# Kernel optimization log

Hardware: AMD Instinct MI355X
Metric: run time of the kernel (lower is better)

Reference implementation:

```python
import jax, jax.numpy as jnp
import numpy as np

B, N, D, H = 8, 1024, 512, 8
DH = D // H  # 64
ALPHA = 0.2  # LeakyReLU slope (args.alpha)
EPS = 1e-6
NEG = -1e9


def layer_norm(x, g, b):
    mean = jnp.mean(x, axis=-1, keepdims=True)
    std = jnp.std(x, axis=-1, keepdims=True)
    return g * (x - mean) / (std + EPS) + b


def setup_inputs() -> dict:
    key = jax.random.key(0)
    ks = jax.random.split(key, 6)
    x = jax.random.normal(ks[0], (B, N, D), dtype=jnp.float32)
    mask = jnp.zeros((B, N), dtype=jnp.int32)  # unused by the block body
    adj = jax.random.randint(ks[1], (B, N, N), 0, 2).astype(jnp.int32)
    W = jax.random.normal(ks[2], (H, D, DH), dtype=jnp.float32) * 0.05
    a_src = jax.random.normal(ks[3], (H, DH), dtype=jnp.float32) * 0.05
    a_dst = jax.random.normal(ks[4], (H, DH), dtype=jnp.float32) * 0.05
    ln1_g = jnp.ones((D,), jnp.float32)
    ln1_b = jnp.zeros((D,), jnp.float32)
    ln2_g = jnp.ones((D,), jnp.float32)
    ln2_b = jnp.zeros((D,), jnp.float32)
    return {"x": x, "mask": mask, "adj": adj, "W": W, "a_src": a_src,
            "a_dst": a_dst, "ln1_g": ln1_g, "ln1_b": ln1_b,
            "ln2_g": ln2_g, "ln2_b": ln2_b}


def ggat(xn, adj, W, a_src, a_dst):
    # multi-head GAT-style attention over dense adjacency (inputP)
    h = jnp.einsum('bnd,hdk->bhnk', xn, W)                 # [B,H,N,DH]
    f_src = jnp.einsum('bhnk,hk->bhn', h, a_src)           # [B,H,N]
    f_dst = jnp.einsum('bhnk,hk->bhn', h, a_dst)
    e = jax.nn.leaky_relu(f_src[..., :, None] + f_dst[..., None, :], ALPHA)
    e = jnp.where(adj[:, None, :, :] > 0, e, NEG)          # mask non-edges
    attn = jax.nn.softmax(e, axis=-1)                      # [B,H,N,N]
    out = jnp.einsum('bhnm,bhmk->bhnk', attn, h)           # aggregate
    out = out.transpose(0, 2, 1, 3).reshape(out.shape[0], out.shape[2], -1)
    return jax.nn.elu(out)                                 # [B,N,D]


def reference(x, mask, adj, W, a_src, a_dst, ln1_g, ln1_b, ln2_g, ln2_b):
    # SublayerConnection: x + dropout(sublayer(norm(x))); dropout = identity (eval)
    xn = layer_norm(x, ln1_g, ln1_b)
    y = x + ggat(xn, adj, W, a_src, a_dst)
    # extra LayerNorm + dropout(identity); module returns (dropout(x), 0)
    y = layer_norm(y, ln2_g, ln2_b)
    return y
```

## Files before the change

kernel.cpp:

```cpp
#include <hip/hip_runtime.h>
#include <stdint.h>

#define B_ 8
#define N_ 1024
#define D_ 512
#define H_ 8
#define DH_ 64


using f16x8 = __attribute__((ext_vector_type(8))) _Float16;
using h2    = __attribute__((ext_vector_type(2))) _Float16;
using f32x4 = __attribute__((ext_vector_type(4))) float;

__device__ __forceinline__ float bf2f(uint32_t u) {
  union { uint32_t u; float f; } c; c.u = u << 16; return c.f;
}
__device__ __forceinline__ uint16_t f2bf(float f) {
  union { float f; uint32_t u; } c; c.f = f;
  return (uint16_t)((c.u + 0x7FFFu + ((c.u >> 16) & 1u)) >> 16);
}
__device__ __forceinline__ uint16_t f2h(float f) {
  union { _Float16 h; uint16_t u; } c; c.h = (_Float16)f; return c.u;
}
__device__ __forceinline__ float h2f(uint16_t u) {
  union { uint16_t u; _Float16 h; } c; c.u = u; return (float)c.h;
}
__device__ __forceinline__ uint32_t pk2h(float a, float b) {
  union { h2 h; uint32_t u; } c; c.h = (h2){(_Float16)a, (_Float16)b}; return c.u;
}
__device__ __forceinline__ h2 u2h2(uint32_t u) {
  union { uint32_t u; h2 h; } c; c.u = u; return c.h;
}
__device__ __forceinline__ uint32_t h22u(h2 h) {
  union { h2 h; uint32_t u; } c; c.h = h; return c.u;
}
__device__ __forceinline__ h2 h2splat(float v) {
  return (h2){(_Float16)v, (_Float16)v};
}
__device__ __forceinline__ h2 hmax2(h2 a, h2 b) {
#if defined(__has_builtin)
#if __has_builtin(__builtin_elementwise_max)
  return __builtin_elementwise_max(a, b);
#else
  h2 r; r.x = a.x > b.x ? a.x : b.x; r.y = a.y > b.y ? a.y : b.y; return r;
#endif
#else
  h2 r; r.x = a.x > b.x ? a.x : b.x; r.y = a.y > b.y ? a.y : b.y; return r;
#endif
}
__device__ __forceinline__ void gload16(const void* g, void* l) {
  __builtin_amdgcn_global_load_lds(
      (const __attribute__((address_space(1))) uint32_t*)g,
      (__attribute__((address_space(3))) uint32_t*)l, 16, 0, 0);
}
__device__ __forceinline__ void load8f(const void* p, size_t idx, int f32, float v[8]) {
  if (f32) {
    const float4* q = (const float4*)((const float*)p + idx);
    float4 a = q[0], b = q[1];
    v[0]=a.x; v[1]=a.y; v[2]=a.z; v[3]=a.w; v[4]=b.x; v[5]=b.y; v[6]=b.z; v[7]=b.w;
  } else {
    uint4 u = *(const uint4*)((const uint16_t*)p + idx);
    const uint32_t* w = (const uint32_t*)&u;
#pragma unroll
    for (int e = 0; e < 4; e++) { v[2*e] = bf2f(w[e] & 0xffffu); v[2*e+1] = bf2f(w[e] >> 16); }
  }
}
__device__ __forceinline__ float load1f(const void* p, size_t idx, int f32) {
  return f32 ? ((const float*)p)[idx] : bf2f(((const uint16_t*)p)[idx]);
}

__device__ __forceinline__ int detect_f32_block(const uint16_t* x, int t, int* sflag) {
  if (t == 0) *sflag = 0;
  __syncthreads();
  uint2 u = ((const uint2*)x)[t];
  uint32_t bad = 0;
  bad |= (((u.x >> 7)  & 0xffu) >= 0x90u);
  bad |= (((u.x >> 23) & 0xffu) >= 0x90u);
  bad |= (((u.y >> 7)  & 0xffu) >= 0x90u);
  bad |= (((u.y >> 23) & 0xffu) >= 0x90u);
  if (__any(bad)) { if ((t & 63) == 0) atomicOr(sflag, 1); }
  __syncthreads();
  return *sflag;
}

__global__ __launch_bounds__(256) void k_pp(const int* __restrict__ adj,
                                            unsigned long long* __restrict__ adjp,
                                            const uint16_t* __restrict__ xr,
                                            int* __restrict__ flag,
                                            const void* __restrict__ x,
                                            const void* __restrict__ g,
                                            const void* __restrict__ bb,
                                            uint16_t* __restrict__ xn,
                                            const void* __restrict__ W,
                                            uint16_t* __restrict__ Wt) {
  const int bx = blockIdx.x, t = threadIdx.x;
  if (bx < 2048) {
    const int row  = bx * 4 + (t >> 6);
    const int lane = t & 63;
    const int* ar = adj + (size_t)row * N_;
#pragma unroll
    for (int c = 0; c < 16; c++) {
      unsigned long long m = __ballot(ar[c * 64 + lane] > 0);
      if (lane == 0) adjp[(size_t)row * 16 + c] = m;
    }
    return;
  }
  __shared__ int sflag;
  if (bx == 2048) {
    int f32 = detect_f32_block(xr, t, &sflag);
    if (t == 0) *flag = f32;
    return;
  }
  if (bx >= 4097) {
    const int f32 = detect_f32_block(xr, t, &sflag);
    const int bw = bx - 4097;
    const int h = bw >> 3, dt = bw & 7;
    __shared__ uint16_t tile[64][65];
    const size_t sbase = ((size_t)h * D_ + dt * 64) * DH_;
    for (int e = t; e < 4096; e += 256) tile[e >> 6][e & 63] = f2h(load1f(W, sbase + e, f32));
    __syncthreads();
    uint16_t* dst = Wt + (size_t)h * DH_ * D_ + dt * 64;
    for (int e = t; e < 4096; e += 256) {
      const int k = e >> 6, dd = e & 63;
      dst[(size_t)k * D_ + dd] = tile[dd][k];
    }
    return;
  }
  const int f32 = detect_f32_block(xr, t, &sflag);
  const int row  = (bx - 2049) * 4 + (t >> 6);
  const int lane = t & 63;
  const size_t base = (size_t)row * D_ + lane * 8;
  float v[8]; load8f(x, base, f32, v);
  float s = 0.f, sq = 0.f;
#pragma unroll
  for (int e = 0; e < 8; e++) { s += v[e]; sq += v[e] * v[e]; }
#pragma unroll
  for (int d = 32; d; d >>= 1) { s += __shfl_xor(s, d); sq += __shfl_xor(sq, d); }
  const float mean = s * (1.0f / D_);
  float var = fmaxf(sq * (1.0f / D_) - mean * mean, 0.0f);
  const float inv = 1.0f / (sqrtf(var) + 1e-6f);
  float gv[8], bv[8];
  load8f(g, lane * 8, f32, gv); load8f(bb, lane * 8, f32, bv);
  uint4 ov; uint32_t* ow = (uint32_t*)&ov;
#pragma unroll
  for (int e = 0; e < 4; e++) {
    float o0 = gv[2*e]   * ((v[2*e]   - mean) * inv) + bv[2*e];
    float o1 = gv[2*e+1] * ((v[2*e+1] - mean) * inv) + bv[2*e+1];
    ow[e] = (uint32_t)f2h(o0) | ((uint32_t)f2h(o1) << 16);
  }
  *(uint4*)(xn + base) = ov;
}

__global__ __launch_bounds__(256, 2) void k_gemm(const uint16_t* __restrict__ xn,
                                              const uint16_t* __restrict__ Wt,
                                              uint16_t* __restrict__ ht,
                                              const void* __restrict__ asr,
                                              const void* __restrict__ adst,
                                              float* __restrict__ fs,
                                              float* __restrict__ fd,
                                              const int* __restrict__ flag) {
  const int h = blockIdx.x;
  const int r0 = blockIdx.y * 64;
  const int t = threadIdx.x;
  const int wv = t >> 6, lane = t & 63, q = lane >> 4, m16 = lane & 15;
  const int wr = wv >> 1, wc = wv & 1;

  __shared__ union {
    struct { __align__(16) uint16_t A[2][64 * 72]; __align__(16) uint16_t Bt[2][64 * 72]; } st;
    __align__(16) uint16_t tr[64 * 72];
  } L;

  f32x4 acc[2][2] = {};
  const int srow = t >> 2, soff = (t & 3) * 16;
  const int o = srow * 72 + soff;
  const uint16_t* gA = xn + (size_t)(r0 + srow) * D_ + soff;
  const uint16_t* gB = Wt + ((size_t)h * DH_ + srow) * D_ + soff;

  uint4 va0 = *(const uint4*)(gA);
  uint4 va1 = *(const uint4*)(gA + 8);
  uint4 vb0 = *(const uint4*)(gB);
  uint4 vb1 = *(const uint4*)(gB + 8);
  *(uint4*)&L.st.A[0][o]      = va0;  *(uint4*)&L.st.A[0][o + 8]  = va1;
  *(uint4*)&L.st.Bt[0][o]     = vb0;  *(uint4*)&L.st.Bt[0][o + 8] = vb1;
  va0 = *(const uint4*)(gA + 64);  va1 = *(const uint4*)(gA + 72);
  vb0 = *(const uint4*)(gB + 64);  vb1 = *(const uint4*)(gB + 72);
  int cur = 0;
  for (int k0 = 0; k0 < D_; k0 += 64) {
    __syncthreads();
    if (k0 + 64 < D_) {
      *(uint4*)&L.st.A[cur ^ 1][o]      = va0;  *(uint4*)&L.st.A[cur ^ 1][o + 8]  = va1;
      *(uint4*)&L.st.Bt[cur ^ 1][o]     = vb0;  *(uint4*)&L.st.Bt[cur ^ 1][o + 8] = vb1;
      if (k0 + 128 < D_) {
        va0 = *(const uint4*)(gA + k0 + 128);  va1 = *(const uint4*)(gA + k0 + 136);
        vb0 = *(const uint4*)(gB + k0 + 128);  vb1 = *(const uint4*)(gB + k0 + 136);
      }
    }
#pragma unroll
    for (int ks = 0; ks < 2; ks++) {
      f16x8 a0 = *(const f16x8*)&L.st.A[cur][(wr * 32 + m16) * 72 + ks * 32 + q * 8];
      f16x8 a1 = *(const f16x8*)&L.st.A[cur][(wr * 32 + 16 + m16) * 72 + ks * 32 + q * 8];
      f16x8 b0 = *(const f16x8*)&L.st.Bt[cur][(wc * 32 + m16) * 72 + ks * 32 + q * 8];
      f16x8 b1 = *(const f16x8*)&L.st.Bt[cur][(wc * 32 + 16 + m16) * 72 + ks * 32 + q * 8];
      acc[0][0] = __builtin_amdgcn_mfma_f32_16x16x32_f16(a0, b0, acc[0][0], 0, 0, 0);
      acc[0][1] = __builtin_amdgcn_mfma_f32_16x16x32_f16(a0, b1, acc[0][1], 0, 0, 0);
      acc[1][0] = __builtin_amdgcn_mfma_f32_16x16x32_f16(a1, b0, acc[1][0], 0, 0, 0);
      acc[1][1] = __builtin_amdgcn_mfma_f32_16x16x32_f16(a1, b1, acc[1][1], 0, 0, 0);
    }
    cur ^= 1;
  }
  __syncthreads();
#pragma unroll
  for (int i2 = 0; i2 < 2; i2++)
#pragma unroll
    for (int j2 = 0; j2 < 2; j2++) {
      f32x4 vv = acc[i2][j2];
      const int sl = wr * 32 + i2 * 16 + q * 4;
      const int kl = wc * 32 + j2 * 16 + m16;
#pragma unroll
      for (int r = 0; r < 4; r++) L.tr[kl * 72 + sl + r] = f2h(vv[r]);
    }
  __syncthreads();
  const int b = r0 >> 10, n0 = r0 & 1023;
  {
    const int k = t >> 2, ns = (t & 3) * 16;
    const size_t base = (((size_t)b * H_ + h) * DH_ + k) * (size_t)N_ + n0 + ns;
    *(uint4*)(ht + base) = *(const uint4*)&L.tr[k * 72 + ns];
    *(uint4*)(ht + base + 8) = *(const uint4*)&L.tr[k * 72 + ns + 8];
  }
  {
    const int f32 = *flag;
    const int nl = t >> 2, qd = (t & 3) * 16;
    float ss = 0.f, sd = 0.f;
#pragma unroll
    for (int dd = 0; dd < 16; dd++) {
      float hv = h2f(L.tr[(qd + dd) * 72 + nl]);
      ss = fmaf(hv, load1f(asr,  h * DH_ + qd + dd, f32), ss);
      sd = fmaf(hv, load1f(adst, h * DH_ + qd + dd, f32), sd);
    }
    ss += __shfl_xor(ss, 1); ss += __shfl_xor(ss, 2);
    sd += __shfl_xor(sd, 1); sd += __shfl_xor(sd, 2);
    if ((t & 3) == 0) {
      fs[((size_t)b * H_ + h) * N_ + n0 + nl] = ss;
      fd[((size_t)b * H_ + h) * N_ + n0 + nl] = sd;
    }
  }
}

__global__ __launch_bounds__(256, 2) void k_attn(const uint16_t* __restrict__ ht,
                                                 const float* __restrict__ fs,
                                                 const float* __restrict__ fd,
                                                 const uint32_t* __restrict__ adjp,
                                                 uint16_t* __restrict__ oat) {
  const int bid = blockIdx.x;
  const int bh = bid & 63, itile = bid >> 6;
  const int b = bh >> 3, h = bh & 7;
  const int i0 = itile * 128;
  const int t = threadIdx.x, wv = t >> 6, lane = t & 63, q = lane >> 4, m16 = lane & 15;
  __shared__ __align__(16) uint16_t Hs[2][64 * 128];
  __shared__ __align__(16) uint32_t E1p[N_ / 2];
  __shared__ __align__(16) uint32_t E2p[N_ / 2];

  const uint16_t* hbase = ht + (size_t)bh * (DH_ * N_);
  int srow[4], soff[4];
#pragma unroll
  for (int i = 0; i < 4; i++) {
    const int r = wv * 16 + i * 4 + (lane >> 4);
    srow[i] = r;
    soff[i] = ((lane & 15) * 8) ^ ((r & 7) << 3);
  }
#define STAGE(jc, buf)                                                         \
  {                                                                            \
    _Pragma("unroll")                                                          \
    for (int ii = 0; ii < 4; ii++) {                                           \
      gload16(hbase + (size_t)srow[ii] * N_ + (jc) + soff[ii],                 \
              &(buf)[(wv * 16 + ii * 4) * 128]);                               \
    }                                                                          \
  }
  STAGE(0, Hs[0]);

  for (int jp = t; jp < N_ / 2; jp += 256) {
    float2 fv = ((const float2*)(fd + (size_t)bh * N_))[jp];
    E1p[jp] = pk2h(exp2f(fv.x * 1.44269504f), exp2f(fv.y * 1.44269504f));
    E2p[jp] = pk2h(exp2f(fv.x * 0.28853901f), exp2f(fv.y * 0.28853901f));
  }
  const int iA0 = i0 + wv * 32 + m16;
  const int iA1 = iA0 + 16;
  const h2 R0 = h2splat(fminf(exp2f(fs[(size_t)bh * N_ + iA0] * -1.15415603f), 60000.f));
  const h2 R1 = h2splat(fminf(exp2f(fs[(size_t)bh * N_ + iA1] * -1.15415603f), 60000.f));
  const uint32_t* arow0 = adjp + ((size_t)b * N_ + iA0) * 32;
  const uint32_t* arow1 = adjp + ((size_t)b * N_ + iA1) * 32;
  union { uint16_t u[8]; f16x8 v; } ones;
#pragma unroll
  for (int e = 0; e < 8; e++) ones.u[e] = 0x3C00u;
  f32x4 acc[2][5] = {};
  const int csw = (m16 & 7) << 3;
  uint4 aw0 = *(const uint4*)(arow0);
  uint4 aw1 = *(const uint4*)(arow1);
  for (int c = 0; c < 8; c++) {
    __syncthreads();
    if (c < 7) STAGE((c + 1) * 128, Hs[(c + 1) & 1]);
    const uint32_t cw0[4] = {aw0.x, aw0.y, aw0.z, aw0.w};
    const uint32_t cw1[4] = {aw1.x, aw1.y, aw1.z, aw1.w};
    if (c < 7) {
      aw0 = *(const uint4*)(arow0 + (c + 1) * 4);
      aw1 = *(const uint4*)(arow1 + (c + 1) * 4);
    }
    const uint16_t* Hc = Hs[c & 1];
    const int eb = c * 64;
#pragma unroll
    for (int s = 0; s < 4; s++) {
      const int js = s * 32;
      const int jb = (js + q * 8) ^ csw;
      f16x8 hf0 = *(const f16x8*)&Hc[(m16)*128      + jb];
      f16x8 hf1 = *(const f16x8*)&Hc[(16 + m16)*128 + jb];
      f16x8 hf2 = *(const f16x8*)&Hc[(32 + m16)*128 + jb];
      f16x8 hf3 = *(const f16x8*)&Hc[(48 + m16)*128 + jb];
      const int ei = eb + s * 16 + q * 4;
      const uint4 e1u = *(const uint4*)&E1p[ei];
      const uint4 e2u = *(const uint4*)&E2p[ei];
      const h2 e1[4] = {u2h2(e1u.x), u2h2(e1u.y), u2h2(e1u.z), u2h2(e1u.w)};
      const h2 e2[4] = {u2h2(e2u.x), u2h2(e2u.y), u2h2(e2u.z), u2h2(e2u.w)};
      const uint32_t ab0 = (cw0[s] >> (q * 8)) & 0xffu;
      const uint32_t ab1 = (cw1[s] >> (q * 8)) & 0xffu;
      const uint32_t t0 = ab0 | (ab0 << 15);
      const uint32_t t1 = ab1 | (ab1 << 15);
#pragma unroll
      for (int f = 0; f < 2; f++) {
        const h2 Rf = f ? R1 : R0;
        const uint32_t tt = f ? t1 : t0;
        union { uint32_t u[4]; f16x8 v; } af;
#pragma unroll
        for (int p = 0; p < 4; p++) {
          h2 pm = hmax2(e1[p], Rf * e2[p]);
          af.u[p] = h22u(pm) & (((tt >> (2 * p)) & 0x10001u) * 0xFFFFu);
        }
        acc[f][0] = __builtin_amdgcn_mfma_f32_16x16x32_f16(af.v, hf0, acc[f][0], 0, 0, 0);
        acc[f][1] = __builtin_amdgcn_mfma_f32_16x16x32_f16(af.v, hf1, acc[f][1], 0, 0, 0);
        acc[f][2] = __builtin_amdgcn_mfma_f32_16x16x32_f16(af.v, hf2, acc[f][2], 0, 0, 0);
        acc[f][3] = __builtin_amdgcn_mfma_f32_16x16x32_f16(af.v, hf3, acc[f][3], 0, 0, 0);
        acc[f][4] = __builtin_amdgcn_mfma_f32_16x16x32_f16(af.v, ones.v, acc[f][4], 0, 0, 0);
      }
    }
  }
#undef STAGE
#pragma unroll
  for (int f = 0; f < 2; f++) {
    float linv[4];
#pragma unroll
    for (int r = 0; r < 4; r++) linv[r] = 1.0f / acc[f][4][r];
    const int ibl = i0 + wv * 32 + f * 16 + q * 4;
#pragma unroll
    for (int nt = 0; nt < 4; nt++)
#pragma unroll
      for (int r = 0; r < 4; r++) {
        oat[((size_t)b * N_ + ibl + r) * D_ + h * DH_ + nt * 16 + m16] =
            f2h(acc[f][nt][r] * linv[r]);
      }
  }
}

__global__ __launch_bounds__(256) void k_final(const void* __restrict__ x,
                                               const uint16_t* __restrict__ oa,
                                               const void* __restrict__ g,
                                               const void* __restrict__ bb,
                                               void* __restrict__ out,
                                               const int* __restrict__ flag) {
  const int f32 = *flag;
  const int row = blockIdx.x * 4 + (threadIdx.x >> 6);
  const int lane = threadIdx.x & 63;
  const size_t base = (size_t)row * D_ + lane * 8;
  float xv[8]; load8f(x, base, f32, xv);
  uint4 av = *(const uint4*)(oa + base);
  const uint32_t* aw = (const uint32_t*)&av;
  float v[8], s = 0.f, sq = 0.f;
#pragma unroll
  for (int e = 0; e < 4; e++) {
    float a0 = h2f((uint16_t)(aw[e] & 0xffffu));
    float a1 = h2f((uint16_t)(aw[e] >> 16));
    a0 = a0 > 0.f ? a0 : exp2f(a0 * 1.44269504f) - 1.0f;
    a1 = a1 > 0.f ? a1 : exp2f(a1 * 1.44269504f) - 1.0f;
    float t0 = xv[2*e] + a0, t1 = xv[2*e+1] + a1;
    v[2*e] = t0; v[2*e+1] = t1;
    s += t0 + t1; sq += t0 * t0 + t1 * t1;
  }
#pragma unroll
  for (int d = 32; d; d >>= 1) { s += __shfl_xor(s, d); sq += __shfl_xor(sq, d); }
  const float mean = s * (1.0f / D_);
  float var = fmaxf(sq * (1.0f / D_) - mean * mean, 0.0f);
  const float inv = 1.0f / (sqrtf(var) + 1e-6f);
  float gv[8], bv[8];
  load8f(g, lane * 8, f32, gv); load8f(bb, lane * 8, f32, bv);
  float r8[8];
#pragma unroll
  for (int e = 0; e < 8; e++) r8[e] = gv[e] * ((v[e] - mean) * inv) + bv[e];
  if (f32) {
    float* o = (float*)out + base;
    float4 o0 = {r8[0], r8[1], r8[2], r8[3]};
    float4 o1 = {r8[4], r8[5], r8[6], r8[7]};
    *(float4*)(o) = o0;
    *(float4*)(o + 4) = o1;
  } else {
    uint4 ov; uint32_t* ow = (uint32_t*)&ov;
#pragma unroll
    for (int e = 0; e < 4; e++)
      ow[e] = (uint32_t)f2bf(r8[2*e]) | ((uint32_t)f2bf(r8[2*e+1]) << 16);
    *(uint4*)((uint16_t*)out + base) = ov;
  }
}

extern "C" void kernel_launch(void* const* d_in, const int* in_sizes, int n_in,
                              void* d_out, int out_size, void* d_ws, size_t ws_size,
                              hipStream_t stream) {
  const void* x = d_in[0];
  const int* adj = (const int*)d_in[2];
  const void* W = d_in[3];
  const void* asr = d_in[4];
  const void* adst = d_in[5];
  const void* g1 = d_in[6];
  const void* b1 = d_in[7];
  const void* g2 = d_in[8];
  const void* b2 = d_in[9];

  uint8_t* ws = (uint8_t*)d_ws;
  uint16_t* ht = (uint16_t*)(ws);
  uint16_t* xn = (uint16_t*)(ws + 8388608);
  uint16_t* oat = xn;
  uint16_t* Wt = (uint16_t*)(ws + 16777216);
  uint32_t* adjp = (uint32_t*)(ws + 17301504);
  float* fs = (float*)(ws + 18350080);
  float* fd = (float*)(ws + 18612224);
  int* flag = (int*)(ws + 18874368);

  k_pp<<<dim3(4161), dim3(256), 0, stream>>>(adj, (unsigned long long*)adjp,
                                             (const uint16_t*)x, flag,
                                             x, g1, b1, xn, W, Wt);
  k_gemm<<<dim3(8, 128), dim3(256), 0, stream>>>(xn, Wt, ht, asr, adst, fs, fd, flag);
  k_attn<<<dim3(512), dim3(256), 0, stream>>>(ht, fs, fd, adjp, oat);
  k_final<<<dim3(2048), dim3(256), 0, stream>>>(x, oat, g2, b2, d_out, flag);
}
```

Before: 157.6 us.

## Give each attention wave 64 query rows, halving the block to two waves

The attention kernel now runs 128 threads (2 waves) per block instead of 256, and each wave handles 64 query rows (4 row fragments) instead of 32. Each LDS-staged H fragment and E1/E2 value is then reused across twice as many MFMAs, which cuts LDS reads per unit of work. Each wave loads twice as much of the tile during staging. The price is double the accumulator registers (80 floats) and fewer waves per CU for hiding latency. The launch bound changes to (128,1) to match.

```diff
diff --git a/kernel.cpp b/kernel.cpp
--- a/kernel.cpp
+++ b/kernel.cpp
@@ -47,6 +47,12 @@
 #else
   h2 r; r.x = a.x > b.x ? a.x : b.x; r.y = a.y > b.y ? a.y : b.y; return r;
 #endif
+}
+__device__ __forceinline__ f16x8 ones_frag() {
+  union { uint16_t u[8]; f16x8 v; } o;
+#pragma unroll
+  for (int e = 0; e < 8; e++) o.u[e] = 0x3C00u;
+  return o.v;
 }
 __device__ __forceinline__ void gload16(const void* g, void* l) {
   __builtin_amdgcn_global_load_lds(
@@ -246,7 +252,7 @@
   }
 }
 
-__global__ __launch_bounds__(256, 2) void k_attn(const uint16_t* __restrict__ ht,
+__global__ __launch_bounds__(128, 1) void k_attn(const uint16_t* __restrict__ ht,
                                                  const float* __restrict__ fs,
                                                  const float* __restrict__ fd,
                                                  const uint32_t* __restrict__ adjp,
@@ -261,49 +267,52 @@
   __shared__ __align__(16) uint32_t E2p[N_ / 2];
 
   const uint16_t* hbase = ht + (size_t)bh * (DH_ * N_);
-  int srow[4], soff[4];
-#pragma unroll
-  for (int i = 0; i < 4; i++) {
-    const int r = wv * 16 + i * 4 + (lane >> 4);
+  int srow[8], soff[8];
+#pragma unroll
+  for (int i = 0; i < 8; i++) {
+    const int r = wv * 32 + i * 4 + (lane >> 4);
     srow[i] = r;
     soff[i] = ((lane & 15) * 8) ^ ((r & 7) << 3);
   }
 #define STAGE(jc, buf)                                                         \
   {                                                                            \
     _Pragma("unroll")                                                          \
-    for (int ii = 0; ii < 4; ii++) {                                           \
+    for (int ii = 0; ii < 8; ii++) {                                           \
       gload16(hbase + (size_t)srow[ii] * N_ + (jc) + soff[ii],                 \
-              &(buf)[(wv * 16 + ii * 4) * 128]);                               \
+              &(buf)[(wv * 32 + ii * 4) * 128]);                               \
     }                                                                          \
   }
   STAGE(0, Hs[0]);
 
-  for (int jp = t; jp < N_ / 2; jp += 256) {
+  for (int jp = t; jp < N_ / 2; jp += 128) {
     float2 fv = ((const float2*)(fd + (size_t)bh * N_))[jp];
     E1p[jp] = pk2h(exp2f(fv.x * 1.44269504f), exp2f(fv.y * 1.44269504f));
     E2p[jp] = pk2h(exp2f(fv.x * 0.28853901f), exp2f(fv.y * 0.28853901f));
   }
-  const int iA0 = i0 + wv * 32 + m16;
-  const int iA1 = iA0 + 16;
-  const h2 R0 = h2splat(fminf(exp2f(fs[(size_t)bh * N_ + iA0] * -1.15415603f), 60000.f));
-  const h2 R1 = h2splat(fminf(exp2f(fs[(size_t)bh * N_ + iA1] * -1.15415603f), 60000.f));
-  const uint32_t* arow0 = adjp + ((size_t)b * N_ + iA0) * 32;
-  const uint32_t* arow1 = adjp + ((size_t)b * N_ + iA1) * 32;
-  union { uint16_t u[8]; f16x8 v; } ones;
-#pragma unroll
-  for (int e = 0; e < 8; e++) ones.u[e] = 0x3C00u;
-  f32x4 acc[2][5] = {};
+  h2 R[4];
+  const uint32_t* arow[4];
+#pragma unroll
+  for (int f = 0; f < 4; f++) {
+    const int iA = i0 + wv * 64 + f * 16 + m16;
+    R[f] = h2splat(fminf(exp2f(fs[(size_t)bh * N_ + iA] * -1.15415603f), 60000.f));
+    arow[f] = adjp + ((size_t)b * N_ + iA) * 32;
+  }
+  f32x4 acc[4][5] = {};
   const int csw = (m16 & 7) << 3;
-  uint4 aw0 = *(const uint4*)(arow0);
-  uint4 aw1 = *(const uint4*)(arow1);
+  uint4 aw[4];
+#pragma unroll
+  for (int f = 0; f < 4; f++) aw[f] = *(const uint4*)(arow[f]);
   for (int c = 0; c < 8; c++) {
     __syncthreads();
     if (c < 7) STAGE((c + 1) * 128, Hs[(c + 1) & 1]);
-    const uint32_t cw0[4] = {aw0.x, aw0.y, aw0.z, aw0.w};
-    const uint32_t cw1[4] = {aw1.x, aw1.y, aw1.z, aw1.w};
+    uint32_t cw[4][4];
+#pragma unroll
+    for (int f = 0; f < 4; f++) {
+      cw[f][0] = aw[f].x; cw[f][1] = aw[f].y; cw[f][2] = aw[f].z; cw[f][3] = aw[f].w;
+    }
     if (c < 7) {
-      aw0 = *(const uint4*)(arow0 + (c + 1) * 4);
-      aw1 = *(const uint4*)(arow1 + (c + 1) * 4);
+#pragma unroll
+      for (int f = 0; f < 4; f++) aw[f] = *(const uint4*)(arow[f] + (c + 1) * 4);
     }
     const uint16_t* Hc = Hs[c & 1];
     const int eb = c * 64;
@@ -320,35 +329,31 @@
       const uint4 e2u = *(const uint4*)&E2p[ei];
       const h2 e1[4] = {u2h2(e1u.x), u2h2(e1u.y), u2h2(e1u.z), u2h2(e1u.w)};
       const h2 e2[4] = {u2h2(e2u.x), u2h2(e2u.y), u2h2(e2u.z), u2h2(e2u.w)};
-      const uint32_t ab0 = (cw0[s] >> (q * 8)) & 0xffu;
-      const uint32_t ab1 = (cw1[s] >> (q * 8)) & 0xffu;
-      const uint32_t t0 = ab0 | (ab0 << 15);
-      const uint32_t t1 = ab1 | (ab1 << 15);
-#pragma unroll
-      for (int f = 0; f < 2; f++) {
-        const h2 Rf = f ? R1 : R0;
-        const uint32_t tt = f ? t1 : t0;
+#pragma unroll
+      for (int f = 0; f < 4; f++) {
+        const uint32_t ab = (cw[f][s] >> (q * 8)) & 0xffu;
+        const uint32_t tt = ab | (ab << 15);
         union { uint32_t u[4]; f16x8 v; } af;
 #pragma unroll
         for (int p = 0; p < 4; p++) {
-          h2 pm = hmax2(e1[p], Rf * e2[p]);
+          h2 pm = hmax2(e1[p], R[f] * e2[p]);
           af.u[p] = h22u(pm) & (((tt >> (2 * p)) & 0x10001u) * 0xFFFFu);
         }
         acc[f][0] = __builtin_amdgcn_mfma_f32_16x16x32_f16(af.v, hf0, acc[f][0], 0, 0, 0);
         acc[f][1] = __builtin_amdgcn_mfma_f32_16x16x32_f16(af.v, hf1, acc[f][1], 0, 0, 0);
         acc[f][2] = __builtin_amdgcn_mfma_f32_16x16x32_f16(af.v, hf2, acc[f][2], 0, 0, 0);
         acc[f][3] = __builtin_amdgcn_mfma_f32_16x16x32_f16(af.v, hf3, acc[f][3], 0, 0, 0);
-        acc[f][4] = __builtin_amdgcn_mfma_f32_16x16x32_f16(af.v, ones.v, acc[f][4], 0, 0, 0);
+        acc[f][4] = __builtin_amdgcn_mfma_f32_16x16x32_f16(af.v, ones_frag(), acc[f][4], 0, 0, 0);
       }
     }
   }
 #undef STAGE
 #pragma unroll
-  for (int f = 0; f < 2; f++) {
+  for (int f = 0; f < 4; f++) {
     float linv[4];
 #pragma unroll
     for (int r = 0; r < 4; r++) linv[r] = 1.0f / acc[f][4][r];
-    const int ibl = i0 + wv * 32 + f * 16 + q * 4;
+    const int ibl = i0 + wv * 64 + f * 16 + q * 4;
 #pragma unroll
     for (int nt = 0; nt < 4; nt++)
 #pragma unroll
@@ -435,6 +440,6 @@
                                              (const uint16_t*)x, flag,
                                              x, g1, b1, xn, W, Wt);
   k_gemm<<<dim3(8, 128), dim3(256), 0, stream>>>(xn, Wt, ht, asr, adst, fs, fd, flag);
-  k_attn<<<dim3(512), dim3(256), 0, stream>>>(ht, fs, fd, adjp, oat);
+  k_attn<<<dim3(512), dim3(128), 0, stream>>>(ht, fs, fd, adjp, oat);
   k_final<<<dim3(2048), dim3(256), 0, stream>>>(x, oat, g2, b2, d_out, flag);
 }
```

New measurement: 160.9 us. 2.1% more time.
